# Kernel tuning notes

Hardware: AMD Instinct MI355X
Metric: run time of the kernel (lower is better)

## Reference

```python
import jax, jax.numpy as jnp
import numpy as np

THETA_BINS = 8
PHI_BINS = 8
BLOCK_SIZE = 15  # odd, per assert
STRIDE = 1       # with stride=1, nr_block along each axis == image dim
EPS = 2.220446049250313e-16  # sys.float_info.epsilon, as in the original


def setup_inputs() -> dict:
    key = jax.random.key(0)
    x = jax.random.normal(key, (96, 96, 96), dtype=jnp.float32)
    return {"x": x}


def _sliding_sum0(a, bs):
    """Sliding-window sum of size bs along axis 0, stride 1, nblocks = a.shape[0].
    Windows extending past the end see zeros (original code indexes past the image;
    we treat out-of-range voxels as zero contribution)."""
    pad = [(0, bs - 1)] + [(0, 0)] * (a.ndim - 1)
    cs = jnp.cumsum(jnp.pad(a, pad), axis=0)
    cs = jnp.concatenate([jnp.zeros_like(cs[:1]), cs], axis=0)  # exclusive prefix
    return cs[bs:] - cs[:-bs]  # out[i] = sum a[i:i+bs]


def reference(x):
    Z, Y, X = x.shape
    Tb, Pb, BS = THETA_BINS, PHI_BINS, BLOCK_SIZE
    B = Tb * Pb

    # conv3d with fixed central-difference kernels, padding=1 (zero pad)
    p = jnp.pad(x, 1)
    gz = p[2:, 1:-1, 1:-1] - p[:-2, 1:-1, 1:-1]
    gy = p[1:-1, 2:, 1:-1] - p[1:-1, :-2, 1:-1]
    gx = p[1:-1, 1:-1, 2:] - p[1:-1, 1:-1, :-2]

    r = jnp.sqrt(gx * gx + gy * gy + gz * gz)
    theta = jnp.arctan(gy / (gx + EPS))          # range (-pi/2, pi/2)
    phi = jnp.arccos(gz / (r + EPS))             # range [0, pi]

    two_pi = jnp.float32(2.0 * np.pi)
    theta = jnp.where(theta < 0, theta + two_pi, theta)  # angle_normalizer(theta,0,2pi)

    t_raw = theta / (two_pi / Tb)
    p_raw = phi / (jnp.float32(np.pi) / Pb)

    lt = jnp.floor(t_raw).astype(jnp.int32)
    lt = jnp.where(lt == Tb, 0, lt)
    lp = jnp.floor(p_raw).astype(jnp.int32)
    lp = jnp.where(lp == Pb, 0, lp)
    ht = (lt + 1) % Tb
    hp = (lp + 1) % Pb

    # NOTE: the original uses the THETA fractional part for the phi ratios too
    # (a bug in the source) - reproduced faithfully here.
    frac = t_raw - jnp.floor(t_raw)
    w_lo = jnp.minimum(frac, 1.0 - frac)   # low-bin ratio per the branchy original
    w_hi = 1.0 - w_lo                      # high-bin ratio
    wp_lo = jnp.where(frac == 0, jnp.float32(1.0), w_lo)  # frac==0 -> phi not split
    wp_hi = 1.0 - wp_lo

    # per-voxel soft-binned histogram volume [N, B] via 4 scatter-adds
    n = r.size
    rows = jnp.arange(n)
    rf = r.reshape(-1)
    ltf, htf = lt.reshape(-1), ht.reshape(-1)
    lpf, hpf = lp.reshape(-1), hp.reshape(-1)
    wlof, whif = w_lo.reshape(-1), w_hi.reshape(-1)
    wplof, wphif = wp_lo.reshape(-1), wp_hi.reshape(-1)

    V = jnp.zeros((n, B), dtype=r.dtype)
    V = V.at[rows, ltf * Pb + lpf].add(rf * wlof * wplof)
    V = V.at[rows, htf * Pb + lpf].add(rf * whif * wplof)
    V = V.at[rows, ltf * Pb + hpf].add(rf * wlof * wphif)
    V = V.at[rows, htf * Pb + hpf].add(rf * whif * wphif)
    V = V.reshape(Z, Y, X, B)

    # block histograms: separable sliding-window sum over block_size^3, stride 1
    for ax in (0, 1, 2):
        V = jnp.moveaxis(_sliding_sum0(jnp.moveaxis(V, ax, 0), BS), 0, ax)

    return V[None, None]  # [1, 1, nbz, nby, nbx, theta_bins*phi_bins]
```

## Files before the change

kernel.cpp:

```cpp
#include <hip/hip_runtime.h>

#define DIM 96
#define NBINS 64
#define BSZ 15
#define PADROWS (DIM + BSZ - 1)
#define C4N 16
#define RS4 17
#define NTHREADS 256
#define STRIPS (NTHREADS / C4N)
#define PPS (DIM / STRIPS)

__global__ __launch_bounds__(NTHREADS) void k_bin_xsum(
    const float* __restrict__ in, float* __restrict__ out)
{
    __shared__ float4 V4[PADROWS * RS4];
    float* Vf = (float*)V4;
    const int tid = threadIdx.x;
    const int y = blockIdx.x;
    const int z = blockIdx.y;

    for (int i = tid; i < PADROWS * RS4; i += NTHREADS)
        V4[i] = make_float4(0.f, 0.f, 0.f, 0.f);
    __syncthreads();

    if (tid < DIM) {
        const int x = tid;
        const int idx = (z * DIM + y) * DIM + x;
        const float xm = (x > 0)       ? in[idx - 1]         : 0.0f;
        const float xp = (x < DIM - 1) ? in[idx + 1]         : 0.0f;
        const float ym = (y > 0)       ? in[idx - DIM]       : 0.0f;
        const float yp = (y < DIM - 1) ? in[idx + DIM]       : 0.0f;
        const float zm = (z > 0)       ? in[idx - DIM * DIM] : 0.0f;
        const float zp = (z < DIM - 1) ? in[idx + DIM * DIM] : 0.0f;
        const float gx = xp - xm, gy = yp - ym, gz = zp - zm;

        const float EPSF  = 2.220446049250313e-16f;
        const float TWOPI = 6.28318530717958647692f;
        const float PIF   = 3.14159265358979323846f;

        const float r = sqrtf(gx * gx + gy * gy + gz * gz);
        float theta = atanf(gy / (gx + EPSF));
        const float phi = acosf(gz / (r + EPSF));
        if (theta < 0.0f) theta += TWOPI;
        const float t_raw = theta / (TWOPI / 8.0f);
        const float p_raw = phi   / (PIF   / 8.0f);
        const float ft = floorf(t_raw);
        const float fp = floorf(p_raw);
        int lt = (int)ft; if (lt == 8) lt = 0;
        int lp = (int)fp; if (lp == 8) lp = 0;
        const int ht = (lt + 1) & 7;
        const int hp = (lp + 1) & 7;
        const float frac  = t_raw - ft;
        const float w_lo  = fminf(frac, 1.0f - frac);
        const float w_hi  = 1.0f - w_lo;
        const float wp_lo = (frac == 0.0f) ? 1.0f : w_lo;
        const float wp_hi = 1.0f - wp_lo;

        float* vrow = Vf + x * (RS4 * 4);
        vrow[lt * 8 + lp] += r * w_lo * wp_lo;
        vrow[ht * 8 + lp] += r * w_hi * wp_lo;
        vrow[lt * 8 + hp] += r * w_lo * wp_hi;
        vrow[ht * 8 + hp] += r * w_hi * wp_hi;
    }
    __syncthreads();

    const int c4    = tid & (C4N - 1);
    const int strip = tid >> 4;
    int pos = strip * PPS;

    float4 s = make_float4(0.f, 0.f, 0.f, 0.f);
    #pragma unroll
    for (int d = 0; d < BSZ; ++d) {
        const float4 v = V4[(pos + d) * RS4 + c4];
        s.x += v.x; s.y += v.y; s.z += v.z; s.w += v.w;
    }
    float4* out4 = (float4*)out;
    const int base = (z * DIM + y) * DIM * C4N;
    out4[base + pos * C4N + c4] = s;
    #pragma unroll
    for (int j = 1; j < PPS; ++j) {
        const float4 a = V4[pos * RS4 + c4];
        const float4 b = V4[(pos + BSZ) * RS4 + c4];
        s.x += b.x - a.x; s.y += b.y - a.y; s.z += b.z - a.z; s.w += b.w - a.w;
        ++pos;
        out4[base + pos * C4N + c4] = s;
    }
}

__global__ __launch_bounds__(NTHREADS) void k_axis_sum(
    float* __restrict__ data, const int mulY, const int stride4)
{
    __shared__ float4 V4[PADROWS * RS4];
    const int tid = threadIdx.x;
    const int base4 = (blockIdx.y * mulY + blockIdx.x) * C4N;
    float4* data4 = (float4*)data;

    for (int i = tid; i < DIM * C4N; i += NTHREADS) {
        const int pos = i >> 4, c4 = i & 15;
        V4[pos * RS4 + c4] = data4[base4 + pos * stride4 + c4];
    }
    for (int i = tid; i < (PADROWS - DIM) * C4N; i += NTHREADS) {
        const int pos = DIM + (i >> 4), c4 = i & 15;
        V4[pos * RS4 + c4] = make_float4(0.f, 0.f, 0.f, 0.f);
    }
    __syncthreads();

    const int c4    = tid & (C4N - 1);
    const int strip = tid >> 4;
    int pos = strip * PPS;

    float4 s = make_float4(0.f, 0.f, 0.f, 0.f);
    #pragma unroll
    for (int d = 0; d < BSZ; ++d) {
        const float4 v = V4[(pos + d) * RS4 + c4];
        s.x += v.x; s.y += v.y; s.z += v.z; s.w += v.w;
    }
    data4[base4 + pos * stride4 + c4] = s;
    #pragma unroll
    for (int j = 1; j < PPS; ++j) {
        const float4 a = V4[pos * RS4 + c4];
        const float4 b = V4[(pos + BSZ) * RS4 + c4];
        s.x += b.x - a.x; s.y += b.y - a.y; s.z += b.z - a.z; s.w += b.w - a.w;
        ++pos;
        data4[base4 + pos * stride4 + c4] = s;
    }
}

extern "C" void kernel_launch(void* const* d_in, const int* in_sizes, int n_in,
                              void* d_out, int out_size, void* d_ws, size_t ws_size,
                              hipStream_t stream) {
    (void)in_sizes; (void)n_in; (void)d_ws; (void)ws_size; (void)out_size;
    const float* x = (const float*)d_in[0];
    float* out = (float*)d_out;

    dim3 grid(DIM, DIM), block(NTHREADS);
    k_bin_xsum<<<grid, block, 0, stream>>>(x, out);
    k_axis_sum<<<grid, block, 0, stream>>>(out, DIM * DIM, DIM * C4N);
    k_axis_sum<<<grid, block, 0, stream>>>(out, DIM, DIM * DIM * C4N);
}
```

Measured before the change: 353.1 us.

## Replace LDS-staged axis sums with streaming register running sums via workspace

Replaces the shared-memory-staged y/z sliding-window kernels with streaming kernels in which each thread walks one line along the axis, keeping a running float4 sum in registers and reading each element twice from global memory. When the workspace is large enough it ping-pongs out->ws->out and splits each line into two halves across blocks for more parallelism. Otherwise it falls back to an in-place single-pass version. The aim is to drop LDS staging and syncs and to coalesce across x, at the cost of extra global reads and much lower grid occupancy (576 or 1152 blocks instead of 9216).

```diff
diff --git a/kernel.cpp b/kernel.cpp
--- a/kernel.cpp
+++ b/kernel.cpp
@@ -7,8 +7,7 @@
 #define C4N 16
 #define RS4 17
 #define NTHREADS 256
-#define STRIPS (NTHREADS / C4N)
-#define PPS (DIM / STRIPS)
+#define PPS 6
 
 __global__ __launch_bounds__(NTHREADS) void k_bin_xsum(
     const float* __restrict__ in, float* __restrict__ out)
@@ -87,54 +86,90 @@
     }
 }
 
-__global__ __launch_bounds__(NTHREADS) void k_axis_sum(
-    float* __restrict__ data, const int mulY, const int stride4)
+__global__ __launch_bounds__(NTHREADS) void k_axis_stream_rr(
+    const float* __restrict__ src, float* __restrict__ dst,
+    const int lineMul, const int stride4)
 {
-    __shared__ float4 V4[PADROWS * RS4];
     const int tid = threadIdx.x;
-    const int base4 = (blockIdx.y * mulY + blockIdx.x) * C4N;
-    float4* data4 = (float4*)data;
-
-    for (int i = tid; i < DIM * C4N; i += NTHREADS) {
-        const int pos = i >> 4, c4 = i & 15;
-        V4[pos * RS4 + c4] = data4[base4 + pos * stride4 + c4];
-    }
-    for (int i = tid; i < (PADROWS - DIM) * C4N; i += NTHREADS) {
-        const int pos = DIM + (i >> 4), c4 = i & 15;
-        V4[pos * RS4 + c4] = make_float4(0.f, 0.f, 0.f, 0.f);
-    }
-    __syncthreads();
-
-    const int c4    = tid & (C4N - 1);
-    const int strip = tid >> 4;
-    int pos = strip * PPS;
+    const int c4 = tid & (C4N - 1);
+    const int xl = tid >> 4;
+    const int x  = blockIdx.x * 16 + xl;
+    const float4* __restrict__ s4 = (const float4*)src;
+    float4* __restrict__ d4 = (float4*)dst;
+    const size_t base4 = (size_t)blockIdx.y * lineMul + (size_t)x * C4N + c4;
+    const int pblk = DIM / gridDim.z;
+    const int p0 = blockIdx.z * pblk;
 
     float4 s = make_float4(0.f, 0.f, 0.f, 0.f);
     #pragma unroll
-    for (int d = 0; d < BSZ; ++d) {
-        const float4 v = V4[(pos + d) * RS4 + c4];
+    for (int j = 0; j < BSZ - 1; ++j) {
+        const float4 v = s4[base4 + (size_t)(p0 + j) * stride4];
         s.x += v.x; s.y += v.y; s.z += v.z; s.w += v.w;
     }
-    data4[base4 + pos * stride4 + c4] = s;
+    #pragma unroll 4
+    for (int i = 0; i < pblk; ++i) {
+        const int p = p0 + i;
+        const size_t ap = base4 + (size_t)p * stride4;
+        if (p + BSZ - 1 < DIM) {
+            const float4 v = s4[ap + (size_t)(BSZ - 1) * stride4];
+            s.x += v.x; s.y += v.y; s.z += v.z; s.w += v.w;
+        }
+        const float4 vsub = s4[ap];
+        d4[ap] = s;
+        s.x -= vsub.x; s.y -= vsub.y; s.z -= vsub.z; s.w -= vsub.w;
+    }
+}
+
+__global__ __launch_bounds__(NTHREADS) void k_axis_stream_ip(
+    float* data, const int lineMul, const int stride4)
+{
+    const int tid = threadIdx.x;
+    const int c4 = tid & (C4N - 1);
+    const int xl = tid >> 4;
+    const int x  = blockIdx.x * 16 + xl;
+    float4* d4 = (float4*)data;
+    const size_t base4 = (size_t)blockIdx.y * lineMul + (size_t)x * C4N + c4;
+
+    float4 s = make_float4(0.f, 0.f, 0.f, 0.f);
     #pragma unroll
-    for (int j = 1; j < PPS; ++j) {
-        const float4 a = V4[pos * RS4 + c4];
-        const float4 b = V4[(pos + BSZ) * RS4 + c4];
-        s.x += b.x - a.x; s.y += b.y - a.y; s.z += b.z - a.z; s.w += b.w - a.w;
-        ++pos;
-        data4[base4 + pos * stride4 + c4] = s;
+    for (int j = 0; j < BSZ - 1; ++j) {
+        const float4 v = d4[base4 + (size_t)j * stride4];
+        s.x += v.x; s.y += v.y; s.z += v.z; s.w += v.w;
+    }
+    #pragma unroll 4
+    for (int p = 0; p < DIM; ++p) {
+        const size_t ap = base4 + (size_t)p * stride4;
+        if (p + BSZ - 1 < DIM) {
+            const float4 v = d4[ap + (size_t)(BSZ - 1) * stride4];
+            s.x += v.x; s.y += v.y; s.z += v.z; s.w += v.w;
+        }
+        const float4 vsub = d4[ap];
+        d4[ap] = s;
+        s.x -= vsub.x; s.y -= vsub.y; s.z -= vsub.z; s.w -= vsub.w;
     }
 }
 
 extern "C" void kernel_launch(void* const* d_in, const int* in_sizes, int n_in,
                               void* d_out, int out_size, void* d_ws, size_t ws_size,
                               hipStream_t stream) {
-    (void)in_sizes; (void)n_in; (void)d_ws; (void)ws_size; (void)out_size;
+    (void)in_sizes; (void)n_in; (void)out_size;
     const float* x = (const float*)d_in[0];
     float* out = (float*)d_out;
+    float* ws = (float*)d_ws;
+    const size_t need = (size_t)DIM * DIM * DIM * NBINS * sizeof(float);
 
-    dim3 grid(DIM, DIM), block(NTHREADS);
-    k_bin_xsum<<<grid, block, 0, stream>>>(x, out);
-    k_axis_sum<<<grid, block, 0, stream>>>(out, DIM * DIM, DIM * C4N);
-    k_axis_sum<<<grid, block, 0, stream>>>(out, DIM, DIM * DIM * C4N);
+    dim3 block(NTHREADS);
+    k_bin_xsum<<<dim3(DIM, DIM), block, 0, stream>>>(x, out);
+
+    if (ws_size >= need) {
+        k_axis_stream_rr<<<dim3(6, DIM, 2), block, 0, stream>>>(
+            out, ws, DIM * DIM * C4N, DIM * C4N);
+        k_axis_stream_rr<<<dim3(6, DIM, 2), block, 0, stream>>>(
+            ws, out, DIM * C4N, DIM * DIM * C4N);
+    } else {
+        k_axis_stream_ip<<<dim3(6, DIM, 1), block, 0, stream>>>(
+            out, DIM * DIM * C4N, DIM * C4N);
+        k_axis_stream_ip<<<dim3(6, DIM, 1), block, 0, stream>>>(
+            out, DIM * C4N, DIM * DIM * C4N);
+    }
 }
```

Result: slower. 457.9 us (+29.7%).

## Replace LDS-staged axis sums with in-place per-thread register sliding windows

Applied to the files above, without the earlier changes.

The two later axis-sum passes no longer stage a full 96-position line in shared memory. Each thread now walks one whole line of one float4 bin group straight from global memory, keeps the running window sum in registers and overwrites the data in place. The 14-row look-ahead lets each position be read before it is written. This drops the shared-memory staging and the barrier, and cuts the launch to 576 blocks. In exchange, each element is read twice from global memory (relying on cache for the trailing read), and the long serial loop per thread with low occupancy may leave memory latency exposed.

```diff
diff --git a/kernel.cpp b/kernel.cpp
--- a/kernel.cpp
+++ b/kernel.cpp
@@ -7,8 +7,7 @@
 #define C4N 16
 #define RS4 17
 #define NTHREADS 256
-#define STRIPS (NTHREADS / C4N)
-#define PPS (DIM / STRIPS)
+#define PPS 6
 
 __global__ __launch_bounds__(NTHREADS) void k_bin_xsum(
     const float* __restrict__ in, float* __restrict__ out)
@@ -87,54 +86,49 @@
     }
 }
 
-__global__ __launch_bounds__(NTHREADS) void k_axis_sum(
-    float* __restrict__ data, const int mulY, const int stride4)
+__global__ __launch_bounds__(NTHREADS) void k_axis_ip(
+    float* data, const int lineMul, const int stride4)
 {
-    __shared__ float4 V4[PADROWS * RS4];
     const int tid = threadIdx.x;
-    const int base4 = (blockIdx.y * mulY + blockIdx.x) * C4N;
-    float4* data4 = (float4*)data;
-
-    for (int i = tid; i < DIM * C4N; i += NTHREADS) {
-        const int pos = i >> 4, c4 = i & 15;
-        V4[pos * RS4 + c4] = data4[base4 + pos * stride4 + c4];
-    }
-    for (int i = tid; i < (PADROWS - DIM) * C4N; i += NTHREADS) {
-        const int pos = DIM + (i >> 4), c4 = i & 15;
-        V4[pos * RS4 + c4] = make_float4(0.f, 0.f, 0.f, 0.f);
-    }
-    __syncthreads();
-
-    const int c4    = tid & (C4N - 1);
-    const int strip = tid >> 4;
-    int pos = strip * PPS;
+    const int c4 = tid & (C4N - 1);
+    const int xl = tid >> 4;
+    const int x  = blockIdx.x * 16 + xl;
+    float4* d4 = (float4*)data;
+    const size_t base = (size_t)blockIdx.y * lineMul + (size_t)x * C4N + c4;
 
     float4 s = make_float4(0.f, 0.f, 0.f, 0.f);
     #pragma unroll
-    for (int d = 0; d < BSZ; ++d) {
-        const float4 v = V4[(pos + d) * RS4 + c4];
+    for (int j = 0; j < BSZ - 1; ++j) {
+        const float4 v = d4[base + (size_t)j * stride4];
         s.x += v.x; s.y += v.y; s.z += v.z; s.w += v.w;
     }
-    data4[base4 + pos * stride4 + c4] = s;
+    #pragma unroll 6
+    for (int p = 0; p <= DIM - BSZ; ++p) {
+        const size_t ap = base + (size_t)p * stride4;
+        const float4 add = d4[ap + (size_t)(BSZ - 1) * stride4];
+        const float4 sub = d4[ap];
+        s.x += add.x; s.y += add.y; s.z += add.z; s.w += add.w;
+        d4[ap] = s;
+        s.x -= sub.x; s.y -= sub.y; s.z -= sub.z; s.w -= sub.w;
+    }
     #pragma unroll
-    for (int j = 1; j < PPS; ++j) {
-        const float4 a = V4[pos * RS4 + c4];
-        const float4 b = V4[(pos + BSZ) * RS4 + c4];
-        s.x += b.x - a.x; s.y += b.y - a.y; s.z += b.z - a.z; s.w += b.w - a.w;
-        ++pos;
-        data4[base4 + pos * stride4 + c4] = s;
+    for (int p = DIM - BSZ + 1; p < DIM; ++p) {
+        const size_t ap = base + (size_t)p * stride4;
+        const float4 sub = d4[ap];
+        d4[ap] = s;
+        s.x -= sub.x; s.y -= sub.y; s.z -= sub.z; s.w -= sub.w;
     }
 }
 
 extern "C" void kernel_launch(void* const* d_in, const int* in_sizes, int n_in,
                               void* d_out, int out_size, void* d_ws, size_t ws_size,
                               hipStream_t stream) {
-    (void)in_sizes; (void)n_in; (void)d_ws; (void)ws_size; (void)out_size;
+    (void)in_sizes; (void)n_in; (void)out_size; (void)d_ws; (void)ws_size;
     const float* x = (const float*)d_in[0];
     float* out = (float*)d_out;
 
-    dim3 grid(DIM, DIM), block(NTHREADS);
-    k_bin_xsum<<<grid, block, 0, stream>>>(x, out);
-    k_axis_sum<<<grid, block, 0, stream>>>(out, DIM * DIM, DIM * C4N);
-    k_axis_sum<<<grid, block, 0, stream>>>(out, DIM, DIM * DIM * C4N);
+    dim3 block(NTHREADS);
+    k_bin_xsum<<<dim3(DIM, DIM), block, 0, stream>>>(x, out);
+    k_axis_ip<<<dim3(6, DIM), block, 0, stream>>>(out, DIM * DIM * C4N, DIM * C4N);
+    k_axis_ip<<<dim3(6, DIM), block, 0, stream>>>(out, DIM * C4N, DIM * DIM * C4N);
 }
```

After: 411.2 us. +16.5%, slower.
